# Performance work log

Hardware: AMD Instinct MI355X
Metric: run time of the kernel (lower is better)

Reference implementation:

```python
import jax, jax.numpy as jnp
import numpy as np

N = 100000   # nodes
E = 1000000  # edges
G = 2000     # graphs
ND = 64      # node_dim (== hidden_dim so per-layer params stack)
ED = 16      # edge_dim
HD = 64      # hidden_dim
L = 4        # num_layers


def setup_inputs() -> dict:
    key = jax.random.key(0)
    ks = jax.random.split(key, 16)
    s = 0.1  # param init scale
    return {
        "x": jax.random.normal(ks[0], (N, ND), jnp.float32),
        "edge_index": jax.random.randint(ks[1], (2, E), 0, N, jnp.int32),
        "edge_attr": jax.random.normal(ks[2], (E, ED), jnp.float32),
        "batch": jnp.sort(jax.random.randint(ks[3], (N,), 0, G, jnp.int32)),
        "t_cond": jax.random.uniform(ks[4], (G,), jnp.float32),
        # per-layer GINEConv params (stacked over L layers)
        "lin_e": jax.random.normal(ks[5], (L, ED, ND), jnp.float32) * s,  # edge_attr -> in_dim
        "W1": jax.random.normal(ks[6], (L, ND, HD), jnp.float32) * s,
        "b1": jnp.zeros((L, HD), jnp.float32),
        "W2": jax.random.normal(ks[7], (L, HD, HD), jnp.float32) * s,
        "b2": jnp.zeros((L, HD), jnp.float32),
        "eps": jnp.zeros((L,), jnp.float32),  # train_eps=True, init 0
        # head: Linear(HD+1 -> HD), ReLU, Linear(HD -> 1)
        "head_W1": jax.random.normal(ks[8], (HD + 1, HD), jnp.float32) * s,
        "head_b1": jnp.zeros((HD,), jnp.float32),
        "head_W2": jax.random.normal(ks[9], (HD, 1), jnp.float32) * s,
        "head_b2": jnp.zeros((1,), jnp.float32),
    }


def reference(x, edge_index, edge_attr, batch, t_cond,
              lin_e, W1, b1, W2, b2, eps,
              head_W1, head_b1, head_W2, head_b2):
    src = edge_index[0]  # x_j (message source)
    dst = edge_index[1]  # x_i (aggregation target)
    for l in range(L):
        # GINEConv: m_ij = ReLU(x_j + Lin(edge_attr)); aggr = sum_j m_ij
        e = edge_attr @ lin_e[l]                      # [E, ND]
        m = jax.nn.relu(x[src] + e)                   # gather + fuse
        aggr = jax.ops.segment_sum(m, dst, num_segments=N)  # scatter-add [N, ND]
        h = (1.0 + eps[l]) * x + aggr
        x = jax.nn.relu(h @ W1[l] + b1[l]) @ W2[l] + b2[l]  # nn_seq MLP
        x = jax.nn.relu(x)  # outer ReLU (dropout off at inference)
    # global mean pool over graphs
    sums = jax.ops.segment_sum(x, batch, num_segments=G)          # [G, HD]
    cnts = jax.ops.segment_sum(jnp.ones((N, 1), x.dtype), batch, num_segments=G)
    pooled = sums / jnp.maximum(cnts, 1.0)
    h = jnp.concatenate([pooled, t_cond[:, None].astype(x.dtype)], axis=-1)  # [G, HD+1]
    out = jax.nn.relu(h @ head_W1 + head_b1) @ head_W2 + head_b2             # [G, 1]
    return out
```

## Files before the change

### kernel.cpp

```cpp
#include <hip/hip_runtime.h>

#define NDIM 64
#define EDIM 16
#define SCAN_BS 256
#define SCAN_TILE 2048

typedef __attribute__((ext_vector_type(8))) short short8;
typedef __attribute__((ext_vector_type(4))) float f32x4;
typedef __attribute__((ext_vector_type(4))) float f4;

#define AS4 __attribute__((address_space(4)))
__device__ inline const AS4 int* cs_i(const int* p) {
    return (const AS4 int*)(unsigned long long)p;
}
__device__ inline const AS4 f4* cs_f4(const float* p) {
    return (const AS4 f4*)(unsigned long long)p;
}

__device__ inline unsigned short f2bf_rne(float f) {
    unsigned int u = __float_as_uint(f);
    unsigned int r = u + 0x7FFFu + ((u >> 16) & 1u);
    return (unsigned short)(r >> 16);
}
__device__ inline float bf2f(unsigned short h) {
    return __uint_as_float(((unsigned int)h) << 16);
}
__device__ inline void cvt8(const float4 v0, const float4 v1, short8& hi, short8& lo) {
    float v[8] = {v0.x, v0.y, v0.z, v0.w, v1.x, v1.y, v1.z, v1.w};
#pragma unroll
    for (int j = 0; j < 8; ++j) {
        unsigned short h = f2bf_rne(v[j]);
        hi[j] = (short)h;
        lo[j] = (short)f2bf_rne(v[j] - bf2f(h));
    }
}


__global__ __launch_bounds__(256) void hist_kernel(const int* __restrict__ edge_index,
                                                   int* __restrict__ deg, int E) {
    int e = blockIdx.x * blockDim.x + threadIdx.x;
    if (e < E) atomicAdd(&deg[edge_index[E + e]], 1);
}

__global__ __launch_bounds__(SCAN_BS) void scan_tile_kernel(const int* __restrict__ deg,
                                                            int* __restrict__ excl,
                                                            int* __restrict__ tsum, int n) {
    __shared__ int sdata[SCAN_BS];
    int base = blockIdx.x * SCAN_TILE + threadIdx.x * 8;
    int v[8]; int s = 0;
#pragma unroll
    for (int j = 0; j < 8; ++j) { int idx = base + j; int val = (idx < n) ? deg[idx] : 0; v[j] = val; s += val; }
    sdata[threadIdx.x] = s;
    __syncthreads();
    for (int off = 1; off < SCAN_BS; off <<= 1) {
        int t = (threadIdx.x >= (unsigned)off) ? sdata[threadIdx.x - off] : 0;
        __syncthreads();
        sdata[threadIdx.x] += t;
        __syncthreads();
    }
    int incl = sdata[threadIdx.x];
    if (threadIdx.x == SCAN_BS - 1) tsum[blockIdx.x] = incl;
    int run = incl - s;
#pragma unroll
    for (int j = 0; j < 8; ++j) { int idx = base + j; if (idx < n) excl[idx] = run; run += v[j]; }
}

__global__ void scan_sums_kernel(int* tsum, int ntiles) {
    if (threadIdx.x == 0 && blockIdx.x == 0) {
        int run = 0;
        for (int i = 0; i < ntiles; ++i) { int t = tsum[i]; tsum[i] = run; run += t; }
    }
}

__global__ __launch_bounds__(256) void scan_add_kernel(int* __restrict__ rowptr,
                                                       const int* __restrict__ tsum,
                                                       int* __restrict__ fillc, int n, int E) {
    int i = blockIdx.x * blockDim.x + threadIdx.x;
    if (i < n) {
        int v = rowptr[i] + tsum[i / SCAN_TILE];
        rowptr[i] = v;
        fillc[i] = v;
    }
    if (i == 0) rowptr[n] = E;
}

__global__ __launch_bounds__(256) void fill_kernel(const int* __restrict__ edge_index,
                                                   int* __restrict__ fillc,
                                                   int* __restrict__ eids, int E) {
    int e = blockIdx.x * blockDim.x + threadIdx.x;
    if (e < E) {
        int d = edge_index[E + e];
        int pos = atomicAdd(&fillc[d], 1);
        eids[pos] = e;
    }
}

__global__ __launch_bounds__(256) void permute_kernel(const int* __restrict__ eids,
                                                      const int* __restrict__ edge_index,
                                                      const float4* __restrict__ ea,
                                                      float4* __restrict__ gea,
                                                      int* __restrict__ srcs,
                                                      int* __restrict__ gdst, int E) {
    int p = blockIdx.x * blockDim.x + threadIdx.x;
    if (p < E) {
        int e = eids[p];
        srcs[p] = edge_index[e];
        gdst[p] = edge_index[E + e];
        float4 r0 = ea[(size_t)e*4+0], r1 = ea[(size_t)e*4+1],
               r2 = ea[(size_t)e*4+2], r3 = ea[(size_t)e*4+3];
        size_t q = (size_t)p * 4;
        gea[q+0] = r0; gea[q+1] = r1; gea[q+2] = r2; gea[q+3] = r3;
    }
}

__global__ __launch_bounds__(256) void init_h_kernel(const float4* __restrict__ x,
                                                     float4* __restrict__ h,
                                                     const float* __restrict__ eps,
                                                     int layer, int n4) {
    float e1 = 1.0f + eps[layer];
    int i = blockIdx.x * blockDim.x + threadIdx.x;
    int stride = gridDim.x * blockDim.x;
    for (; i < n4; i += stride) {
        float4 v = x[i];
        v.x *= e1; v.y *= e1; v.z *= e1; v.w *= e1;
        h[i] = v;
    }
}

#define EDGE_FMA16(m, A0, A1, A2, A3)                                   \
    m = fmaf(A0.x, le[ 0], m); m = fmaf(A0.y, le[ 1], m);               \
    m = fmaf(A0.z, le[ 2], m); m = fmaf(A0.w, le[ 3], m);               \
    m = fmaf(A1.x, le[ 4], m); m = fmaf(A1.y, le[ 5], m);               \
    m = fmaf(A1.z, le[ 6], m); m = fmaf(A1.w, le[ 7], m);               \
    m = fmaf(A2.x, le[ 8], m); m = fmaf(A2.y, le[ 9], m);               \
    m = fmaf(A2.z, le[10], m); m = fmaf(A2.w, le[11], m);               \
    m = fmaf(A3.x, le[12], m); m = fmaf(A3.y, le[13], m);               \
    m = fmaf(A3.z, le[14], m); m = fmaf(A3.w, le[15], m);


__global__ __launch_bounds__(256) void aggr_flat_kernel(
    const float* __restrict__ xin, float* __restrict__ hacc,
    const int* __restrict__ srcs, const int* __restrict__ gdst,
    const float* __restrict__ gea,
    const float* __restrict__ lin_e, int layer, int E)
{
    const int lane = threadIdx.x & 63;
    float le[16];
    const float* lep = lin_e + (size_t)layer * EDIM * NDIM;
#pragma unroll
    for (int j = 0; j < EDIM; ++j) le[j] = lep[j * NDIM + lane];

    const AS4 int* sc = cs_i(srcs);
    const AS4 int* dc = cs_i(gdst);

    int w = (blockIdx.x * blockDim.x + threadIdx.x) >> 6;
    int W = (gridDim.x * blockDim.x) >> 6;
    int S = (E + W - 1) / W;
    int p    = __builtin_amdgcn_readfirstlane(w * S);
    int pend = __builtin_amdgcn_readfirstlane(min(E, p + S));
    if (p >= pend) return;

    float aggr = 0.0f;
    int dprev = dc[p];
    for (; p + 4 <= pend; p += 4) {
        int s0 = sc[p], s1 = sc[p+1], s2 = sc[p+2], s3 = sc[p+3];
        int d0 = dc[p], d1 = dc[p+1], d2 = dc[p+2], d3 = dc[p+3];
        float xs0 = xin[(size_t)s0 * NDIM + lane];
        float xs1 = xin[(size_t)s1 * NDIM + lane];
        float xs2 = xin[(size_t)s2 * NDIM + lane];
        float xs3 = xin[(size_t)s3 * NDIM + lane];
        const AS4 f4* ea = cs_f4(gea + (size_t)p * EDIM);
        f4 a0 = ea[ 0], a1 = ea[ 1], a2 = ea[ 2], a3 = ea[ 3];
        f4 e0 = ea[ 4], e1 = ea[ 5], e2 = ea[ 6], e3 = ea[ 7];
        f4 c0 = ea[ 8], c1 = ea[ 9], c2 = ea[10], c3 = ea[11];
        f4 g0 = ea[12], g1 = ea[13], g2 = ea[14], g3 = ea[15];
        float m0 = xs0, m1 = xs1, m2 = xs2, m3 = xs3;
        EDGE_FMA16(m0, a0, a1, a2, a3)
        EDGE_FMA16(m1, e0, e1, e2, e3)
        EDGE_FMA16(m2, c0, c1, c2, c3)
        EDGE_FMA16(m3, g0, g1, g2, g3)
        m0 = fmaxf(m0, 0.0f); m1 = fmaxf(m1, 0.0f);
        m2 = fmaxf(m2, 0.0f); m3 = fmaxf(m3, 0.0f);
        if (d3 == dprev) {
            aggr += (m0 + m1) + (m2 + m3);
        } else {
            if (d0 != dprev) { atomicAdd(&hacc[(size_t)dprev * NDIM + lane], aggr); aggr = 0.0f; dprev = d0; }
            aggr += m0;
            if (d1 != dprev) { atomicAdd(&hacc[(size_t)dprev * NDIM + lane], aggr); aggr = 0.0f; dprev = d1; }
            aggr += m1;
            if (d2 != dprev) { atomicAdd(&hacc[(size_t)dprev * NDIM + lane], aggr); aggr = 0.0f; dprev = d2; }
            aggr += m2;
            if (d3 != dprev) { atomicAdd(&hacc[(size_t)dprev * NDIM + lane], aggr); aggr = 0.0f; dprev = d3; }
            aggr += m3;
        }
    }
    for (; p < pend; ++p) {
        int s0 = sc[p];
        int d0 = dc[p];
        float xs0 = xin[(size_t)s0 * NDIM + lane];
        const AS4 f4* ea = cs_f4(gea + (size_t)p * EDIM);
        f4 a0 = ea[0], a1 = ea[1], a2 = ea[2], a3 = ea[3];
        float m0 = xs0;
        EDGE_FMA16(m0, a0, a1, a2, a3)
        if (d0 != dprev) { atomicAdd(&hacc[(size_t)dprev * NDIM + lane], aggr); aggr = 0.0f; dprev = d0; }
        aggr += fmaxf(m0, 0.0f);
    }
    atomicAdd(&hacc[(size_t)dprev * NDIM + lane], aggr);
}


__global__ __launch_bounds__(256) void mlp_mfma_kernel(
    float* __restrict__ h,
    const float* __restrict__ W1, const float* __restrict__ b1,
    const float* __restrict__ W2, const float* __restrict__ b2,
    int layer, int n_nodes)
{
    __shared__ unsigned short sW1hi[4096], sW1lo[4096], sW2hi[4096], sW2lo[4096];
    __shared__ float sY[4][16 * 64];

    const float* w1 = W1 + (size_t)layer * 4096;
    const float* w2 = W2 + (size_t)layer * 4096;
    for (int idx = threadIdx.x; idx < 4096; idx += 256) {
        int k = idx >> 6, n = idx & 63;
        int c = k >> 5, q = (k >> 3) & 3, j = k & 7;
        int fidx = ((c * 4 + q) * 64 + n) * 8 + j;
        float a = w1[idx];
        unsigned short hi = f2bf_rne(a);
        sW1hi[fidx] = hi;
        sW1lo[fidx] = f2bf_rne(a - bf2f(hi));
        float b = w2[idx];
        hi = f2bf_rne(b);
        sW2hi[fidx] = hi;
        sW2lo[fidx] = f2bf_rne(b - bf2f(hi));
    }
    __syncthreads();

    const int lane = threadIdx.x & 63;
    const int wid = threadIdx.x >> 6;
    const int m = lane & 15, q = lane >> 4;
    float* Y = sY[wid];

    float b1v[4], b2v[4];
#pragma unroll
    for (int nt = 0; nt < 4; ++nt) {
        b1v[nt] = b1[layer * 64 + m + nt * 16];
        b2v[nt] = b2[layer * 64 + m + nt * 16];
    }

    int tiles = (n_nodes + 15) >> 4;
    int gw = blockIdx.x * 4 + wid;
    int nw = gridDim.x * 4;
    for (int t = gw; t < tiles; t += nw) {
        int r0 = t << 4;
        int rA = r0 + m; if (rA > n_nodes - 1) rA = n_nodes - 1;
        const float* hrow = h + (size_t)rA * 64;

        short8 Ahi[2], Alo[2];
#pragma unroll
        for (int c = 0; c < 2; ++c) {
            const float4* hp = (const float4*)(hrow + c * 32 + q * 8);
            float4 v0 = hp[0], v1 = hp[1];
            cvt8(v0, v1, Ahi[c], Alo[c]);
        }

#pragma unroll
        for (int nt = 0; nt < 4; ++nt) {
            int col = m + nt * 16;
            f32x4 acc = {0.f, 0.f, 0.f, 0.f};
#pragma unroll
            for (int c = 0; c < 2; ++c) {
                short8 bh = *(const short8*)&sW1hi[((c * 4 + q) * 64 + col) * 8];
                short8 bl = *(const short8*)&sW1lo[((c * 4 + q) * 64 + col) * 8];
                acc = __builtin_amdgcn_mfma_f32_16x16x32_bf16(Ahi[c], bh, acc, 0, 0, 0);
                acc = __builtin_amdgcn_mfma_f32_16x16x32_bf16(Alo[c], bh, acc, 0, 0, 0);
                acc = __builtin_amdgcn_mfma_f32_16x16x32_bf16(Ahi[c], bl, acc, 0, 0, 0);
            }
#pragma unroll
            for (int i = 0; i < 4; ++i) {
                int row = q * 4 + i;
                float y = fmaxf(acc[i] + b1v[nt], 0.0f);
                int gran = ((m >> 2) + 4 * nt) ^ row;
                Y[(row << 6) + (gran << 2) + (m & 3)] = y;
            }
        }
        __asm__ volatile("s_waitcnt lgkmcnt(0)" ::: "memory");

        short8 Yhi[2], Ylo[2];
#pragma unroll
        for (int c = 0; c < 2; ++c) {
            int g0 = c * 8 + q * 2;
            float4 v0 = *(const float4*)&Y[(m << 6) + ((g0 ^ m) << 2)];
            float4 v1 = *(const float4*)&Y[(m << 6) + (((g0 + 1) ^ m) << 2)];
            cvt8(v0, v1, Yhi[c], Ylo[c]);
        }

#pragma unroll
        for (int nt = 0; nt < 4; ++nt) {
            int col = m + nt * 16;
            f32x4 acc = {0.f, 0.f, 0.f, 0.f};
#pragma unroll
            for (int c = 0; c < 2; ++c) {
                short8 bh = *(const short8*)&sW2hi[((c * 4 + q) * 64 + col) * 8];
                short8 bl = *(const short8*)&sW2lo[((c * 4 + q) * 64 + col) * 8];
                acc = __builtin_amdgcn_mfma_f32_16x16x32_bf16(Yhi[c], bh, acc, 0, 0, 0);
                acc = __builtin_amdgcn_mfma_f32_16x16x32_bf16(Ylo[c], bh, acc, 0, 0, 0);
                acc = __builtin_amdgcn_mfma_f32_16x16x32_bf16(Yhi[c], bl, acc, 0, 0, 0);
            }
#pragma unroll
            for (int i = 0; i < 4; ++i) {
                int row = r0 + q * 4 + i;
                if (row < n_nodes)
                    h[(size_t)row * 64 + col] = fmaxf(acc[i] + b2v[nt], 0.0f);
            }
        }
    }
}

__global__ __launch_bounds__(256) void layer_kernel(
    const float* __restrict__ xin, float* __restrict__ xout,
    const int* __restrict__ rowptr, const int* __restrict__ eids,
    const int* __restrict__ edge_index,
    const float* __restrict__ edge_attr,
    const float* __restrict__ lin_e, const float* __restrict__ W1, const float* __restrict__ b1,
    const float* __restrict__ W2, const float* __restrict__ b2, const float* __restrict__ eps,
    int layer, int n_nodes, int E)
{
    __shared__ float s_W1[NDIM * NDIM];
    __shared__ float s_W2[NDIM * NDIM];
    const float* w1 = W1 + (size_t)layer * NDIM * NDIM;
    const float* w2 = W2 + (size_t)layer * NDIM * NDIM;
    for (int i = threadIdx.x; i < NDIM * NDIM; i += 256) { s_W1[i] = w1[i]; s_W2[i] = w2[i]; }
    const int lane = threadIdx.x & 63;
    float le[16];
    const float* lep = lin_e + (size_t)layer * EDIM * NDIM;
#pragma unroll
    for (int j = 0; j < EDIM; ++j) le[j] = lep[j * NDIM + lane];
    const float bb1 = b1[layer * NDIM + lane];
    const float bb2 = b2[layer * NDIM + lane];
    const float eps1 = 1.0f + eps[layer];
    __syncthreads();
    int gw = (blockIdx.x * blockDim.x + threadIdx.x) >> 6;
    int nw = (gridDim.x * blockDim.x) >> 6;
    for (int node = gw; node < n_nodes; node += nw) {
        int p0 = rowptr[node], p1 = rowptr[node + 1];
        float aggr = 0.0f;
        for (int p = p0; p < p1; ++p) {
            int e = eids[p];
            int s = edge_index[e];
            float xs = xin[(size_t)s * NDIM + lane];
            const float4* ea = (const float4*)(edge_attr + (size_t)e * EDIM);
            float4 a0 = ea[0], a1 = ea[1], a2 = ea[2], a3 = ea[3];
            float m0 = xs;
            EDGE_FMA16(m0, a0, a1, a2, a3)
            aggr += fmaxf(m0, 0.0f);
        }
        float h = fmaf(eps1, xin[(size_t)node * NDIM + lane], aggr);
        float o1 = bb1;
#pragma unroll 8
        for (int k = 0; k < NDIM; ++k) o1 = fmaf(__shfl(h, k), s_W1[k * NDIM + lane], o1);
        o1 = fmaxf(o1, 0.0f);
        float o2 = bb2;
#pragma unroll 8
        for (int k = 0; k < NDIM; ++k) o2 = fmaf(__shfl(o1, k), s_W2[k * NDIM + lane], o2);
        xout[(size_t)node * NDIM + lane] = fmaxf(o2, 0.0f);
    }
}


__global__ __launch_bounds__(256) void starts_kernel(const int* __restrict__ batch,
                                                     int* __restrict__ starts, int N, int G) {
    int g = blockIdx.x * blockDim.x + threadIdx.x;
    if (g <= G) {
        int lo = 0, hi = N;
        while (lo < hi) { int mid = (lo + hi) >> 1; if (batch[mid] < g) lo = mid + 1; else hi = mid; }
        starts[g] = lo;
    }
}

__global__ __launch_bounds__(256) void poolhead_kernel(const float* __restrict__ x,
                                                       const int* __restrict__ starts,
                                                       const float* __restrict__ t_cond,
                                                       const float* __restrict__ hW1,
                                                       const float* __restrict__ hb1,
                                                       const float* __restrict__ hW2,
                                                       const float* __restrict__ hb2,
                                                       float* __restrict__ out, int G) {
    __shared__ float sW1[(NDIM + 1) * NDIM];
    __shared__ float sb1[NDIM];
    __shared__ float sW2[NDIM];
    for (int i = threadIdx.x; i < (NDIM + 1) * NDIM; i += 256) sW1[i] = hW1[i];
    if (threadIdx.x < NDIM) { sb1[threadIdx.x] = hb1[threadIdx.x]; sW2[threadIdx.x] = hW2[threadIdx.x]; }
    __syncthreads();
    const int lane = threadIdx.x & 63;
    int gw = (blockIdx.x * blockDim.x + threadIdx.x) >> 6;
    int nw = (gridDim.x * blockDim.x) >> 6;
    for (int g = gw; g < G; g += nw) {
        int a = starts[g], b = starts[g + 1];
        float s0 = 0.0f, s1 = 0.0f, s2 = 0.0f, s3 = 0.0f;
        int n = a;
        for (; n + 4 <= b; n += 4) {
            s0 += x[(size_t)n * NDIM + lane];
            s1 += x[(size_t)(n + 1) * NDIM + lane];
            s2 += x[(size_t)(n + 2) * NDIM + lane];
            s3 += x[(size_t)(n + 3) * NDIM + lane];
        }
        for (; n < b; ++n) s0 += x[(size_t)n * NDIM + lane];
        float c = fmaxf((float)(b - a), 1.0f);
        float p = ((s0 + s1) + (s2 + s3)) / c;
        float t = t_cond[g];
        float o1 = fmaf(t, sW1[NDIM * NDIM + lane], sb1[lane]);
#pragma unroll 8
        for (int k = 0; k < NDIM; ++k) o1 = fmaf(__shfl(p, k), sW1[k * NDIM + lane], o1);
        o1 = fmaxf(o1, 0.0f);
        float v = o1 * sW2[lane];
        for (int off = 32; off > 0; off >>= 1) v += __shfl_down(v, off);
        if (lane == 0) out[g] = v + hb2[0];
    }
}


extern "C" void kernel_launch(void* const* d_in, const int* in_sizes, int n_in,
                              void* d_out, int out_size, void* d_ws, size_t ws_size,
                              hipStream_t stream) {
    const float* x_in      = (const float*)d_in[0];
    const int*   edge_index= (const int*)  d_in[1];
    const float* edge_attr = (const float*)d_in[2];
    const int*   batch     = (const int*)  d_in[3];
    const float* t_cond    = (const float*)d_in[4];
    const float* lin_e     = (const float*)d_in[5];
    const float* W1        = (const float*)d_in[6];
    const float* b1        = (const float*)d_in[7];
    const float* W2        = (const float*)d_in[8];
    const float* b2        = (const float*)d_in[9];
    const float* eps       = (const float*)d_in[10];
    const float* hW1       = (const float*)d_in[11];
    const float* hb1       = (const float*)d_in[12];
    const float* hW2       = (const float*)d_in[13];
    const float* hb2       = (const float*)d_in[14];
    float* out = (float*)d_out;

    const int N = in_sizes[3];
    const int E = in_sizes[1] / 2;
    const int G = in_sizes[4];
    const int L = in_sizes[10];
    const int ntiles = (N + SCAN_TILE - 1) / SCAN_TILE;

    char* p = (char*)d_ws;
    auto alloc = [&](size_t bytes) { char* r = p; p += (bytes + 255) & ~(size_t)255; return r; };
    int*   rowptr = (int*)  alloc((size_t)(N + 1) * 4);
    int*   fillc  = (int*)  alloc((size_t)N * 4);
    int*   srcs   = (int*)  alloc((size_t)E * 4);
    int*   gdst   = (int*)  alloc((size_t)E * 4);
    int*   tsum   = (int*)  alloc((size_t)ntiles * 4);
    int*   starts = (int*)  alloc((size_t)(G + 1) * 4);
    float* bufA   = (float*)alloc((size_t)N * NDIM * 4);
    float* bufB   = (float*)alloc((size_t)N * NDIM * 4);
    size_t base_used = (size_t)(p - (char*)d_ws);
    float* gea    = (float*)alloc((size_t)E * EDIM * 4);
    bool use_gea = (base_used + (size_t)E * EDIM * 4) <= ws_size
                   && (size_t)E * 4 <= (size_t)N * NDIM * 4;
    int* eids = (int*)bufA;

    hipMemsetAsync(fillc, 0, (size_t)N * 4, stream);
    hist_kernel<<<(E + 255) / 256, 256, 0, stream>>>(edge_index, fillc, E);
    scan_tile_kernel<<<ntiles, SCAN_BS, 0, stream>>>(fillc, rowptr, tsum, N);
    scan_sums_kernel<<<1, 64, 0, stream>>>(tsum, ntiles);
    scan_add_kernel<<<(N + 255) / 256, 256, 0, stream>>>(rowptr, tsum, fillc, N, E);
    fill_kernel<<<(E + 255) / 256, 256, 0, stream>>>(edge_index, fillc, eids, E);
    if (use_gea) {
        permute_kernel<<<(E + 255) / 256, 256, 0, stream>>>(eids, edge_index, (const float4*)edge_attr,
                                                            (float4*)gea, srcs, gdst, E);
    }
    starts_kernel<<<(G + 256) / 256, 256, 0, stream>>>(batch, starts, N, G);

    const int n4 = N * NDIM / 4;
    const float* cur = x_in;
    float* work = bufA;
    for (int l = 0; l < L; ++l) {
        if (use_gea) {
            init_h_kernel<<<2048, 256, 0, stream>>>((const float4*)cur, (float4*)work, eps, l, n4);
            aggr_flat_kernel<<<2048, 256, 0, stream>>>(cur, work, srcs, gdst, gea, lin_e, l, E);
            mlp_mfma_kernel<<<1024, 256, 0, stream>>>(work, W1, b1, W2, b2, l, N);
            cur = work;
            work = (work == bufA) ? bufB : bufA;
        } else {
            float* tgt = (l == 0) ? bufB : work;
            layer_kernel<<<1024, 256, 0, stream>>>(cur, tgt, rowptr, eids, edge_index,
                                                   edge_attr, lin_e, W1, b1, W2, b2, eps, l, N, E);
            cur = tgt;
            work = (tgt == bufA) ? bufB : bufA;
        }
    }

    poolhead_kernel<<<512, 256, 0, stream>>>(cur, starts, t_cond, hW1, hb1, hW2, hb2, out, G);
}
```

Measured before the change: 699.0 us.

## Store permuted edge attributes as bf16 and fuse next-layer h init into MLP

Permuted edge attributes are now packed as bf16 pairs, which halves the bytes the aggregation kernel streams per edge, and are unpacked with shifts and masks before the FMAs. The MLP kernel also writes (1+eps_next)*x into the other buffer for the next layer, so the per-layer init_h kernel launch and its extra read of x go away. The fill kernel uses a nontemporal store for eids. In exchange, edge features lose precision to bf16 rounding, and the MLP epilogue does an additional full-size store.

```diff
diff --git a/kernel.cpp b/kernel.cpp
--- a/kernel.cpp
+++ b/kernel.cpp
@@ -8,14 +8,18 @@
 typedef __attribute__((ext_vector_type(8))) short short8;
 typedef __attribute__((ext_vector_type(4))) float f32x4;
 typedef __attribute__((ext_vector_type(4))) float f4;
+typedef __attribute__((ext_vector_type(4))) unsigned int u32x4;
 
 #define AS4 __attribute__((address_space(4)))
 __device__ inline const AS4 int* cs_i(const int* p) {
     return (const AS4 int*)(unsigned long long)p;
 }
-__device__ inline const AS4 f4* cs_f4(const float* p) {
-    return (const AS4 f4*)(unsigned long long)p;
-}
+__device__ inline const AS4 u32x4* cs_u4(const unsigned int* p) {
+    return (const AS4 u32x4*)(unsigned long long)p;
+}
+
+#define BF_LO(u) __uint_as_float((u) << 16)
+#define BF_HI(u) __uint_as_float((u) & 0xffff0000u)
 
 __device__ inline unsigned short f2bf_rne(float f) {
     unsigned int u = __float_as_uint(f);
@@ -24,6 +28,9 @@
 }
 __device__ inline float bf2f(unsigned short h) {
     return __uint_as_float(((unsigned int)h) << 16);
+}
+__device__ inline unsigned int pack2(float a, float b) {
+    return (unsigned int)f2bf_rne(a) | ((unsigned int)f2bf_rne(b) << 16);
 }
 __device__ inline void cvt8(const float4 v0, const float4 v1, short8& hi, short8& lo) {
     float v[8] = {v0.x, v0.y, v0.z, v0.w, v1.x, v1.y, v1.z, v1.w};
@@ -91,14 +98,14 @@
     if (e < E) {
         int d = edge_index[E + e];
         int pos = atomicAdd(&fillc[d], 1);
-        eids[pos] = e;
+        __builtin_nontemporal_store(e, &eids[pos]);
     }
 }
 
 __global__ __launch_bounds__(256) void permute_kernel(const int* __restrict__ eids,
                                                       const int* __restrict__ edge_index,
                                                       const float4* __restrict__ ea,
-                                                      float4* __restrict__ gea,
+                                                      u32x4* __restrict__ gea,
                                                       int* __restrict__ srcs,
                                                       int* __restrict__ gdst, int E) {
     int p = blockIdx.x * blockDim.x + threadIdx.x;
@@ -108,8 +115,12 @@
         gdst[p] = edge_index[E + e];
         float4 r0 = ea[(size_t)e*4+0], r1 = ea[(size_t)e*4+1],
                r2 = ea[(size_t)e*4+2], r3 = ea[(size_t)e*4+3];
-        size_t q = (size_t)p * 4;
-        gea[q+0] = r0; gea[q+1] = r1; gea[q+2] = r2; gea[q+3] = r3;
+        u32x4 d0, d1;
+        d0.x = pack2(r0.x, r0.y); d0.y = pack2(r0.z, r0.w);
+        d0.z = pack2(r1.x, r1.y); d0.w = pack2(r1.z, r1.w);
+        d1.x = pack2(r2.x, r2.y); d1.y = pack2(r2.z, r2.w);
+        d1.z = pack2(r3.x, r3.y); d1.w = pack2(r3.z, r3.w);
+        gea[(size_t)p*2+0] = d0; gea[(size_t)p*2+1] = d1;
     }
 }
 
@@ -127,6 +138,16 @@
     }
 }
 
+#define EDGE_FMA16B(m, U0, U1)                                          \
+    m = fmaf(BF_LO(U0.x), le[ 0], m); m = fmaf(BF_HI(U0.x), le[ 1], m); \
+    m = fmaf(BF_LO(U0.y), le[ 2], m); m = fmaf(BF_HI(U0.y), le[ 3], m); \
+    m = fmaf(BF_LO(U0.z), le[ 4], m); m = fmaf(BF_HI(U0.z), le[ 5], m); \
+    m = fmaf(BF_LO(U0.w), le[ 6], m); m = fmaf(BF_HI(U0.w), le[ 7], m); \
+    m = fmaf(BF_LO(U1.x), le[ 8], m); m = fmaf(BF_HI(U1.x), le[ 9], m); \
+    m = fmaf(BF_LO(U1.y), le[10], m); m = fmaf(BF_HI(U1.y), le[11], m); \
+    m = fmaf(BF_LO(U1.z), le[12], m); m = fmaf(BF_HI(U1.z), le[13], m); \
+    m = fmaf(BF_LO(U1.w), le[14], m); m = fmaf(BF_HI(U1.w), le[15], m);
+
 #define EDGE_FMA16(m, A0, A1, A2, A3)                                   \
     m = fmaf(A0.x, le[ 0], m); m = fmaf(A0.y, le[ 1], m);               \
     m = fmaf(A0.z, le[ 2], m); m = fmaf(A0.w, le[ 3], m);               \
@@ -141,7 +162,7 @@
 __global__ __launch_bounds__(256) void aggr_flat_kernel(
     const float* __restrict__ xin, float* __restrict__ hacc,
     const int* __restrict__ srcs, const int* __restrict__ gdst,
-    const float* __restrict__ gea,
+    const unsigned int* __restrict__ gea,
     const float* __restrict__ lin_e, int layer, int E)
 {
     const int lane = threadIdx.x & 63;
@@ -169,16 +190,14 @@
         float xs1 = xin[(size_t)s1 * NDIM + lane];
         float xs2 = xin[(size_t)s2 * NDIM + lane];
         float xs3 = xin[(size_t)s3 * NDIM + lane];
-        const AS4 f4* ea = cs_f4(gea + (size_t)p * EDIM);
-        f4 a0 = ea[ 0], a1 = ea[ 1], a2 = ea[ 2], a3 = ea[ 3];
-        f4 e0 = ea[ 4], e1 = ea[ 5], e2 = ea[ 6], e3 = ea[ 7];
-        f4 c0 = ea[ 8], c1 = ea[ 9], c2 = ea[10], c3 = ea[11];
-        f4 g0 = ea[12], g1 = ea[13], g2 = ea[14], g3 = ea[15];
+        const AS4 u32x4* ea = cs_u4(gea + (size_t)p * 8);
+        u32x4 a0 = ea[0], a1 = ea[1], b0 = ea[2], b1 = ea[3];
+        u32x4 c0 = ea[4], c1 = ea[5], g0 = ea[6], g1 = ea[7];
         float m0 = xs0, m1 = xs1, m2 = xs2, m3 = xs3;
-        EDGE_FMA16(m0, a0, a1, a2, a3)
-        EDGE_FMA16(m1, e0, e1, e2, e3)
-        EDGE_FMA16(m2, c0, c1, c2, c3)
-        EDGE_FMA16(m3, g0, g1, g2, g3)
+        EDGE_FMA16B(m0, a0, a1)
+        EDGE_FMA16B(m1, b0, b1)
+        EDGE_FMA16B(m2, c0, c1)
+        EDGE_FMA16B(m3, g0, g1)
         m0 = fmaxf(m0, 0.0f); m1 = fmaxf(m1, 0.0f);
         m2 = fmaxf(m2, 0.0f); m3 = fmaxf(m3, 0.0f);
         if (d3 == dprev) {
@@ -198,10 +217,10 @@
         int s0 = sc[p];
         int d0 = dc[p];
         float xs0 = xin[(size_t)s0 * NDIM + lane];
-        const AS4 f4* ea = cs_f4(gea + (size_t)p * EDIM);
-        f4 a0 = ea[0], a1 = ea[1], a2 = ea[2], a3 = ea[3];
+        const AS4 u32x4* ea = cs_u4(gea + (size_t)p * 8);
+        u32x4 a0 = ea[0], a1 = ea[1];
         float m0 = xs0;
-        EDGE_FMA16(m0, a0, a1, a2, a3)
+        EDGE_FMA16B(m0, a0, a1)
         if (d0 != dprev) { atomicAdd(&hacc[(size_t)dprev * NDIM + lane], aggr); aggr = 0.0f; dprev = d0; }
         aggr += fmaxf(m0, 0.0f);
     }
@@ -213,6 +232,7 @@
     float* __restrict__ h,
     const float* __restrict__ W1, const float* __restrict__ b1,
     const float* __restrict__ W2, const float* __restrict__ b2,
+    const float* __restrict__ eps, int next_layer, float* __restrict__ hnext,
     int layer, int n_nodes)
 {
     __shared__ unsigned short sW1hi[4096], sW1lo[4096], sW2hi[4096], sW2lo[4096];
@@ -240,6 +260,8 @@
     const int m = lane & 15, q = lane >> 4;
     float* Y = sY[wid];
 
+    const float e1n = (next_layer >= 0) ? (1.0f + eps[next_layer]) : 0.0f;
+
     float b1v[4], b2v[4];
 #pragma unroll
     for (int nt = 0; nt < 4; ++nt) {
@@ -309,8 +331,11 @@
 #pragma unroll
             for (int i = 0; i < 4; ++i) {
                 int row = r0 + q * 4 + i;
-                if (row < n_nodes)
-                    h[(size_t)row * 64 + col] = fmaxf(acc[i] + b2v[nt], 0.0f);
+                if (row < n_nodes) {
+                    float v = fmaxf(acc[i] + b2v[nt], 0.0f);
+                    h[(size_t)row * 64 + col] = v;
+                    if (next_layer >= 0) hnext[(size_t)row * 64 + col] = e1n * v;
+                }
             }
         }
     }
@@ -456,8 +481,8 @@
     float* bufA   = (float*)alloc((size_t)N * NDIM * 4);
     float* bufB   = (float*)alloc((size_t)N * NDIM * 4);
     size_t base_used = (size_t)(p - (char*)d_ws);
-    float* gea    = (float*)alloc((size_t)E * EDIM * 4);
-    bool use_gea = (base_used + (size_t)E * EDIM * 4) <= ws_size
+    unsigned int* gea = (unsigned int*)alloc((size_t)E * 8 * 4);
+    bool use_gea = (base_used + (size_t)E * 8 * 4) <= ws_size
                    && (size_t)E * 4 <= (size_t)N * NDIM * 4;
     int* eids = (int*)bufA;
 
@@ -469,28 +494,35 @@
     fill_kernel<<<(E + 255) / 256, 256, 0, stream>>>(edge_index, fillc, eids, E);
     if (use_gea) {
         permute_kernel<<<(E + 255) / 256, 256, 0, stream>>>(eids, edge_index, (const float4*)edge_attr,
-                                                            (float4*)gea, srcs, gdst, E);
+                                                            (u32x4*)gea, srcs, gdst, E);
     }
     starts_kernel<<<(G + 256) / 256, 256, 0, stream>>>(batch, starts, N, G);
 
     const int n4 = N * NDIM / 4;
-    const float* cur = x_in;
-    float* work = bufA;
-    for (int l = 0; l < L; ++l) {
-        if (use_gea) {
-            init_h_kernel<<<2048, 256, 0, stream>>>((const float4*)cur, (float4*)work, eps, l, n4);
-            aggr_flat_kernel<<<2048, 256, 0, stream>>>(cur, work, srcs, gdst, gea, lin_e, l, E);
-            mlp_mfma_kernel<<<1024, 256, 0, stream>>>(work, W1, b1, W2, b2, l, N);
-            cur = work;
-            work = (work == bufA) ? bufB : bufA;
-        } else {
+    if (use_gea) {
+        const float* xin = x_in;
+        float* hacc  = bufA;
+        float* other = bufB;
+        init_h_kernel<<<2048, 256, 0, stream>>>((const float4*)x_in, (float4*)hacc, eps, 0, n4);
+        for (int l = 0; l < L; ++l) {
+            aggr_flat_kernel<<<2048, 256, 0, stream>>>(xin, hacc, srcs, gdst, gea, lin_e, l, E);
+            int nl = (l + 1 < L) ? l + 1 : -1;
+            mlp_mfma_kernel<<<1024, 256, 0, stream>>>(hacc, W1, b1, W2, b2,
+                                                      eps, nl, other, l, N);
+            xin = hacc;
+            float* t = hacc; hacc = other; other = t;
+        }
+        poolhead_kernel<<<512, 256, 0, stream>>>(xin, starts, t_cond, hW1, hb1, hW2, hb2, out, G);
+    } else {
+        const float* cur = x_in;
+        float* work = bufB;
+        for (int l = 0; l < L; ++l) {
             float* tgt = (l == 0) ? bufB : work;
             layer_kernel<<<1024, 256, 0, stream>>>(cur, tgt, rowptr, eids, edge_index,
                                                    edge_attr, lin_e, W1, b1, W2, b2, eps, l, N, E);
             cur = tgt;
             work = (tgt == bufA) ? bufB : bufA;
         }
-    }
-
-    poolhead_kernel<<<512, 256, 0, stream>>>(cur, starts, t_cond, hW1, hb1, hW2, hb2, out, G);
-}
+        poolhead_kernel<<<512, 256, 0, stream>>>(cur, starts, t_cond, hW1, hb1, hW2, hb2, out, G);
+    }
+}
```

Result: faster. 683.8 us (-2.2%).
